# Optimization experiments

Measured on AMD Instinct MI355X. Metric: run time of the kernel, lower is better.

## Reference

```python
import jax, jax.numpy as jnp
import numpy as np

H = 32       # num query heads
KVH = 8      # num kv heads
HD = 64      # head_dim
ROPE_BASE = 10000.0


def _rope_cos_sin(seq_len, dtype):
    # inv_freq over half the head dim, emb = cat(freqs, freqs)
    inv_freq = 1.0 / (ROPE_BASE ** (jnp.arange(0, HD, 2, dtype=jnp.float32) / HD))
    t = jnp.arange(seq_len, dtype=jnp.float32)
    freqs = t[:, None] * inv_freq[None, :]          # (S, HD/2)
    emb = jnp.concatenate([freqs, freqs], axis=-1)  # (S, HD)
    return jnp.cos(emb).astype(dtype), jnp.sin(emb).astype(dtype)


def _rotate(x):
    x1, x2 = x[..., : HD // 2], x[..., HD // 2 :]
    return jnp.concatenate([-x2, x1], axis=-1)


def setup_inputs() -> dict:
    key = jax.random.key(0)
    ks = jax.random.split(key, 9)
    B, T, D = 2, 2048, 2048
    kv_dim = KVH * HD
    s = 0.02
    return {
        "x": jax.random.normal(ks[0], (B, T, D), jnp.float32),
        "Wq": jax.random.normal(ks[1], (D, D), jnp.float32) * s,
        "bq": jax.random.normal(ks[2], (D,), jnp.float32) * s,
        "Wk": jax.random.normal(ks[3], (kv_dim, D), jnp.float32) * s,
        "bk": jax.random.normal(ks[4], (kv_dim,), jnp.float32) * s,
        "Wv": jax.random.normal(ks[5], (kv_dim, D), jnp.float32) * s,
        "bv": jax.random.normal(ks[6], (kv_dim,), jnp.float32) * s,
        "Wo": jax.random.normal(ks[7], (D, D), jnp.float32) * s,
        "bo": jax.random.normal(ks[8], (D,), jnp.float32) * s,
    }


def reference(x, Wq, bq, Wk, bk, Wv, bv, Wo, bo):
    B, T, D = x.shape
    S = T  # self-attention, no KV cache (offset = 0)

    # QKV projections
    q = (x @ Wq.T + bq).reshape(B, T, H, HD)
    k = (x @ Wk.T + bk).reshape(B, S, KVH, HD)
    v = (x @ Wv.T + bv).reshape(B, S, KVH, HD)

    # RoPE (rotary dim == head_dim, offset 0)
    cos, sin = _rope_cos_sin(S, q.dtype)
    cos = cos[None, :, None, :]  # (1, S, 1, HD)
    sin = sin[None, :, None, :]
    q = q * cos + _rotate(q) * sin
    k = k * cos + _rotate(k) * sin

    # GQA: repeat kv heads (repeat_interleave along head dim)
    r = H // KVH
    k = jnp.repeat(k, r, axis=2)  # (B, S, H, HD)
    v = jnp.repeat(v, r, axis=2)

    # causal scaled dot-product attention
    scale = 1.0 / np.sqrt(HD)
    scores = jnp.einsum("bthd,bshd->bhts", q, k) * scale  # (B, H, T, S)
    causal = jnp.tril(jnp.ones((T, S), dtype=bool))
    scores = jnp.where(causal[None, None], scores, jnp.finfo(scores.dtype).min)
    probs = jax.nn.softmax(scores.astype(jnp.float32), axis=-1).astype(q.dtype)
    attn = jnp.einsum("bhts,bshd->bthd", probs, v)  # (B, T, H, HD)

    out = attn.reshape(B, T, H * HD) @ Wo.T + bo
    return out
```

## Files before the change

### kernel.cpp

```cpp
#include <hip/hip_runtime.h>
#include <hip/hip_bf16.h>
#include <cstdint>

#define B_ 2
#define T_ 2048
#define D_ 2048
#define H_ 32
#define KVH_ 8
#define HD_ 64
#define NQKV_ 3072
#define M_ 4096

typedef __attribute__((ext_vector_type(8))) __bf16 bf16x8;
typedef __attribute__((ext_vector_type(4))) float f32x4;
typedef __attribute__((ext_vector_type(4))) uint32_t u32x4;

__device__ __forceinline__ uint16_t f2bf(float f) {
  uint32_t u = __builtin_bit_cast(uint32_t, f);
  return (uint16_t)((u + 0x7FFFu + ((u >> 16) & 1u)) >> 16);
}

__device__ __forceinline__ uint32_t cvt_pk(float lo, float hi) {
  uint32_t r;
  asm("v_cvt_pk_bf16_f32 %0, %1, %2" : "=v"(r) : "v"(lo), "v"(hi));
  return r;
}

__device__ __forceinline__ void gload_lds16(const void* g, void* l) {
  __builtin_amdgcn_global_load_lds(
      (const __attribute__((address_space(1))) void*)(uintptr_t)g,
      (__attribute__((address_space(3))) void*)(uintptr_t)l, 16, 0, 0);
}

__global__ void cvt_bf16_k(const float* __restrict__ in, uint16_t* __restrict__ out, int n) {
  int i = (blockIdx.x * 256 + threadIdx.x) * 8;
  if (i >= n) return;
  float4 a = *reinterpret_cast<const float4*>(in + i);
  float4 b = *reinterpret_cast<const float4*>(in + i + 4);
  uint4 v;
  v.x = (uint32_t)f2bf(a.x) | ((uint32_t)f2bf(a.y) << 16);
  v.y = (uint32_t)f2bf(a.z) | ((uint32_t)f2bf(a.w) << 16);
  v.z = (uint32_t)f2bf(b.x) | ((uint32_t)f2bf(b.y) << 16);
  v.w = (uint32_t)f2bf(b.z) | ((uint32_t)f2bf(b.w) << 16);
  *reinterpret_cast<uint4*>(out + i) = v;
}

__global__ void concat_bias_k(const float* __restrict__ bq, const float* __restrict__ bk,
                              const float* __restrict__ bv, float* __restrict__ out) {
  int i = blockIdx.x * 256 + threadIdx.x;
  if (i >= NQKV_) return;
  out[i] = (i < D_) ? bq[i] : (i < D_ + 512) ? bk[i - D_] : bv[i - D_ - 512];
}

__global__ void rope_tab_k(float* __restrict__ cosT, float* __restrict__ sinT) {
  int i = blockIdx.x * 256 + threadIdx.x;
  int d = i & 31;
  int t = i >> 5;
  float inv = expf(-(float)d * (1.0f / 32.0f) * logf(10000.0f));
  float f = (float)t * inv;
  cosT[i] = cosf(f);
  sinT[i] = sinf(f);
}

#define BM 128
#define BN 128
#define BK 64
__global__ __launch_bounds__(256, 2)
void gemm_bf16(const uint16_t* __restrict__ A, const uint16_t* __restrict__ Bw,
               const float* __restrict__ bias, float* __restrict__ C,
               int M, int N, int K) {
  __shared__ __align__(16) uint16_t As[BM * BK];
  __shared__ __align__(16) uint16_t Bs[BN * BK];
  const int tid = threadIdx.x;
  const int lane = tid & 63;
  const int w = tid >> 6;
  const int wm = w >> 1, wn = w & 1;
  const int l16 = lane & 15, lq = lane >> 4;

  int lin = blockIdx.y * gridDim.x + blockIdx.x;
  int qn = (gridDim.x * gridDim.y) >> 3;
  int swz = (lin & 7) * qn + (lin >> 3);
  const int m0 = (swz / gridDim.x) * BM, n0 = (swz % gridDim.x) * BN;

  f32x4 acc[4][4] = {};

  for (int k0 = 0; k0 < K; k0 += BK) {
#pragma unroll
    for (int r = 0; r < 4; ++r) {
      int idx = r * 256 + tid;
      int row = idx >> 3;
      int c8 = (idx & 7) ^ (row & 7);
      gload_lds16(A + (size_t)(m0 + row) * K + k0 + c8 * 8, &As[idx * 8]);
    }
#pragma unroll
    for (int r = 0; r < 4; ++r) {
      int idx = r * 256 + tid;
      int row = idx >> 3;
      int c8 = (idx & 7) ^ (row & 7);
      gload_lds16(Bw + (size_t)(n0 + row) * K + k0 + c8 * 8, &Bs[idx * 8]);
    }
    __syncthreads();
#pragma unroll
    for (int ks = 0; ks < 2; ++ks) {
      bf16x8 av[4], bv[4];
      int k8 = ks * 4 + lq;
#pragma unroll
      for (int mi = 0; mi < 4; ++mi) {
        int row = wm * 64 + mi * 16 + l16;
        av[mi] = *reinterpret_cast<const bf16x8*>(&As[row * BK + ((k8 ^ (row & 7)) * 8)]);
      }
#pragma unroll
      for (int ni = 0; ni < 4; ++ni) {
        int row = wn * 64 + ni * 16 + l16;
        bv[ni] = *reinterpret_cast<const bf16x8*>(&Bs[row * BK + ((k8 ^ (row & 7)) * 8)]);
      }
#pragma unroll
      for (int mi = 0; mi < 4; ++mi)
#pragma unroll
        for (int ni = 0; ni < 4; ++ni)
          acc[mi][ni] = __builtin_amdgcn_mfma_f32_16x16x32_bf16(av[mi], bv[ni], acc[mi][ni], 0, 0, 0);
    }
    __syncthreads();
  }

#pragma unroll
  for (int mi = 0; mi < 4; ++mi) {
    int r0 = m0 + wm * 64 + mi * 16 + lq * 4;
#pragma unroll
    for (int ni = 0; ni < 4; ++ni) {
      int c = n0 + wn * 64 + ni * 16 + l16;
      float bb = bias[c];
#pragma unroll
      for (int rr = 0; rr < 4; ++rr)
        C[(size_t)(r0 + rr) * N + c] = acc[mi][ni][rr] + bb;
    }
  }
}

__global__ void rope_qk_k(const float* __restrict__ QKV, const float* __restrict__ cosT,
                          const float* __restrict__ sinT, uint16_t* __restrict__ qb,
                          uint16_t* __restrict__ kb) {
  int tid = blockIdx.x * 256 + threadIdx.x;
  int d = tid & 31;
  int t = (tid >> 5) & (T_ - 1);
  int rest = tid >> 16;
  int hh = rest % 40;
  int b = rest / 40;
  const float PREQ = 0.125f * 1.44269504f;
  float c = cosT[t * 32 + d];
  float s = sinT[t * 32 + d];
  size_t rowoff = (size_t)(b * T_ + t) * NQKV_;
  const int lq = d >> 3, e = d & 7;
  const int l16 = t & 15;
  const int lofs = (lq * 16 + l16) * 8 + e;
  if (hh < H_) {
    const float* q = QKV + rowoff + hh * 64;
    float x1 = q[d], x2 = q[d + 32];
    int tile = t >> 5, mf = (t >> 4) & 1;
    size_t base = ((size_t)(b * H_ + hh) * 64 + tile) * 2048;
    qb[base + (0 * 2 + mf) * 512 + lofs] = f2bf((x1 * c - x2 * s) * PREQ);
    qb[base + (1 * 2 + mf) * 512 + lofs] = f2bf((x2 * c + x1 * s) * PREQ);
  } else {
    int kh = hh - H_;
    const float* kp = QKV + rowoff + D_ + kh * 64;
    float x1 = kp[d], x2 = kp[d + 32];
    int it = t >> 6, nf = (t >> 4) & 3;
    size_t base = (size_t)(b * KVH_ + kh) * (T_ * HD_) + (size_t)it * 4096;
    kb[base + (0 * 8 + nf) * 512 + lofs] = f2bf(x1 * c - x2 * s);
    kb[base + (4 + nf) * 512 + lofs] = f2bf(x2 * c + x1 * s);
  }
}

__global__ void cvt_v_k(const float* __restrict__ QKV, uint16_t* __restrict__ vt) {
  int tid = blockIdx.x * 256 + threadIdx.x;
  int t8 = tid & 255;
  int rest = tid >> 8;
  int b = rest >> 9;
  int col = 2560 + (rest & 511);
  int d = rest & 63;
  int kvh = (rest >> 6) & 7;
  uint16_t tmp[8];
#pragma unroll
  for (int i = 0; i < 8; ++i)
    tmp[i] = f2bf(QKV[(size_t)(b * T_ + t8 * 8 + i) * NQKV_ + col]);
  uint4 v;
  v.x = (uint32_t)tmp[0] | ((uint32_t)tmp[1] << 16);
  v.y = (uint32_t)tmp[2] | ((uint32_t)tmp[3] << 16);
  v.z = (uint32_t)tmp[4] | ((uint32_t)tmp[5] << 16);
  v.w = (uint32_t)tmp[6] | ((uint32_t)tmp[7] << 16);
  int it = t8 >> 3, k2 = (t8 >> 2) & 1, lq = t8 & 3;
  int dn = d >> 4, l16 = d & 15;
  size_t base = (size_t)(b * KVH_ + kvh) * (T_ * HD_);
  *reinterpret_cast<uint4*>(vt + base + ((size_t)(it * 2 + k2) * 4 + dn) * 512 +
                            (lq * 16 + l16) * 8) = v;
}

__global__ __launch_bounds__(256, 2)
void flash_attn_k(const uint16_t* __restrict__ qb, const uint16_t* __restrict__ kb,
                  const uint16_t* __restrict__ vt, uint16_t* __restrict__ ob) {
  __shared__ __align__(16) uint16_t P_lds[4][32 * 72];
  const int lane = threadIdx.x & 63;
  const int w = threadIdx.x >> 6;
  const int l16 = lane & 15, lq = lane >> 4;
  const int bh = (blockIdx.x & 15) * 4 + w;
  const int rank = blockIdx.x >> 4;
  const int pair = rank & 31;
  const int tile = (rank & 32) ? (63 - pair) : pair;
  const int b = bh >> 5, h = bh & 31;
  const int kvh = h >> 2;
  uint16_t* P = P_lds[w];

  const uint16_t* Qp = qb + ((size_t)(b * H_ + h) * 64 + tile) * 2048;
  const uint16_t* Kp = kb + (size_t)(b * KVH_ + kvh) * (T_ * HD_);
  const uint16_t* Vp = vt + (size_t)(b * KVH_ + kvh) * (T_ * HD_);
  const int lofs = lane * 8;

  const int q0 = tile * 32;
  u32x4 ones_u = {0x3F803F80u, 0x3F803F80u, 0x3F803F80u, 0x3F803F80u};
  bf16x8 ones = __builtin_bit_cast(bf16x8, ones_u);

  bf16x8 aq[2][2];
#pragma unroll
  for (int mf = 0; mf < 2; ++mf)
#pragma unroll
    for (int ks = 0; ks < 2; ++ks)
      aq[mf][ks] = *reinterpret_cast<const bf16x8*>(Qp + (ks * 2 + mf) * 512 + lofs);

  f32x4 acc[2][4] = {};
  f32x4 acc_l[2] = {};

  const int nt = (tile >> 1) + 1;

  bf16x8 kA[2][4], kB[2][4];
#pragma unroll
  for (int ks = 0; ks < 2; ++ks)
#pragma unroll
    for (int nf = 0; nf < 4; ++nf)
      kA[ks][nf] = *reinterpret_cast<const bf16x8*>(Kp + (ks * 4 + nf) * 512 + lofs);

#define FLASH_STEP(KCUR, KNXT, IT)                                                     \
  do {                                                                                 \
    const int kv0 = (IT) * 64;                                                         \
    f32x4 sacc[4][2] = {};                                                             \
    _Pragma("unroll")                                                                  \
    for (int ks = 0; ks < 2; ++ks)                                                     \
      _Pragma("unroll")                                                                \
      for (int nf = 0; nf < 4; ++nf)                                                   \
        _Pragma("unroll")                                                              \
        for (int mf = 0; mf < 2; ++mf)                                                 \
          sacc[nf][mf] = __builtin_amdgcn_mfma_f32_16x16x32_bf16(                      \
              KCUR[ks][nf], aq[mf][ks], sacc[nf][mf], 0, 0, 0);                        \
    const int itn = ((IT) + 1 < nt) ? (IT) + 1 : (IT);                                 \
    _Pragma("unroll")                                                                  \
    for (int ks = 0; ks < 2; ++ks)                                                     \
      _Pragma("unroll")                                                                \
      for (int nf = 0; nf < 4; ++nf)                                                   \
        KNXT[ks][nf] = *reinterpret_cast<const bf16x8*>(                               \
            Kp + ((size_t)(itn * 2 + ks) * 4 + nf) * 512 + lofs);                      \
    bf16x8 vv[2][4];                                                                   \
    _Pragma("unroll")                                                                  \
    for (int k2 = 0; k2 < 2; ++k2)                                                     \
      _Pragma("unroll")                                                                \
      for (int dn = 0; dn < 4; ++dn)                                                   \
        vv[k2][dn] = *reinterpret_cast<const bf16x8*>(                                 \
            Vp + ((size_t)((IT) * 2 + k2) * 4 + dn) * 512 + lofs);                     \
    if ((IT) == nt - 1) {                                                              \
      _Pragma("unroll")                                                                \
      for (int mf = 0; mf < 2; ++mf) {                                                 \
        int qg = q0 + mf * 16 + l16;                                                   \
        _Pragma("unroll")                                                              \
        for (int nf = 0; nf < 4; ++nf)                                                 \
          _Pragma("unroll")                                                            \
          for (int r = 0; r < 4; ++r)                                                  \
            if (kv0 + nf * 16 + lq * 4 + r > qg) sacc[nf][mf][r] = -1e30f;             \
      }                                                                                \
    }                                                                                  \
    _Pragma("unroll")                                                                  \
    for (int mf = 0; mf < 2; ++mf) {                                                   \
      uint16_t* rowp = P + (mf * 16 + l16) * 72;                                       \
      _Pragma("unroll")                                                                \
      for (int nf = 0; nf < 4; ++nf) {                                                 \
        float p0 = __builtin_amdgcn_exp2f(sacc[nf][mf][0]);                            \
        float p1 = __builtin_amdgcn_exp2f(sacc[nf][mf][1]);                            \
        float p2 = __builtin_amdgcn_exp2f(sacc[nf][mf][2]);                            \
        float p3 = __builtin_amdgcn_exp2f(sacc[nf][mf][3]);                            \
        uint2 pk;                                                                      \
        pk.x = cvt_pk(p0, p1);                                                         \
        pk.y = cvt_pk(p2, p3);                                                         \
        *reinterpret_cast<uint2*>(rowp + nf * 16 + lq * 4) = pk;                       \
      }                                                                                \
    }                                                                                  \
    bf16x8 pa[2][2];                                                                   \
    _Pragma("unroll")                                                                  \
    for (int mf = 0; mf < 2; ++mf)                                                     \
      _Pragma("unroll")                                                                \
      for (int k2 = 0; k2 < 2; ++k2)                                                   \
        pa[mf][k2] = *reinterpret_cast<const bf16x8*>(                                 \
            P + (mf * 16 + l16) * 72 + k2 * 32 + lq * 8);                              \
    _Pragma("unroll")                                                                  \
    for (int k2 = 0; k2 < 2; ++k2)                                                     \
      _Pragma("unroll")                                                                \
      for (int mf = 0; mf < 2; ++mf) {                                                 \
        acc_l[mf] = __builtin_amdgcn_mfma_f32_16x16x32_bf16(ones, pa[mf][k2],          \
                                                            acc_l[mf], 0, 0, 0);      \
        _Pragma("unroll")                                                              \
        for (int dn = 0; dn < 4; ++dn)                                                 \
          acc[mf][dn] = __builtin_amdgcn_mfma_f32_16x16x32_bf16(                       \
              vv[k2][dn], pa[mf][k2], acc[mf][dn], 0, 0, 0);                           \
      }                                                                                \
  } while (0)

  {
    int it = 0;
    for (;;) {
      FLASH_STEP(kA, kB, it);
      ++it;
      if (it == nt) break;
      FLASH_STEP(kB, kA, it);
      ++it;
      if (it == nt) break;
    }
  }
#undef FLASH_STEP

#pragma unroll
  for (int mf = 0; mf < 2; ++mf) {
    float inv = 1.0f / acc_l[mf][0];
    uint16_t* rowp = P + (mf * 16 + l16) * 72;
#pragma unroll
    for (int dn = 0; dn < 4; ++dn) {
      uint2 pk;
      pk.x = cvt_pk(acc[mf][dn][0] * inv, acc[mf][dn][1] * inv);
      pk.y = cvt_pk(acc[mf][dn][2] * inv, acc[mf][dn][3] * inv);
      *reinterpret_cast<uint2*>(rowp + dn * 16 + lq * 4) = pk;
    }
  }
  {
    int orow = lane >> 1, ohalf = (lane & 1) * 32;
    uint16_t* op = ob + (size_t)(b * T_ + q0 + orow) * D_ + h * HD_ + ohalf;
    const uint16_t* lp = P + orow * 72 + ohalf;
#pragma unroll
    for (int j = 0; j < 4; ++j)
      *reinterpret_cast<uint4*>(op + j * 8) = *reinterpret_cast<const uint4*>(lp + j * 8);
  }
}

extern "C" void kernel_launch(void* const* d_in, const int* in_sizes, int n_in,
                              void* d_out, int out_size, void* d_ws, size_t ws_size,
                              hipStream_t stream) {
  const float* x  = (const float*)d_in[0];
  const float* Wq = (const float*)d_in[1];
  const float* bq = (const float*)d_in[2];
  const float* Wk = (const float*)d_in[3];
  const float* bk = (const float*)d_in[4];
  const float* Wv = (const float*)d_in[5];
  const float* bv = (const float*)d_in[6];
  const float* Wo = (const float*)d_in[7];
  const float* bo = (const float*)d_in[8];
  float* out = (float*)d_out;

  char* ws = (char*)d_ws;
  size_t off = 0;
  auto alloc = [&](size_t bytes) {
    void* p = ws + off;
    off += (bytes + 255) & ~(size_t)255;
    return p;
  };
  uint16_t* xb    = (uint16_t*)alloc((size_t)M_ * D_ * 2);
  uint16_t* wqkv  = (uint16_t*)alloc((size_t)NQKV_ * D_ * 2);
  uint16_t* wo_b  = (uint16_t*)alloc((size_t)D_ * D_ * 2);
  float*    bqkv  = (float*)alloc(NQKV_ * 4);
  float*    cosT  = (float*)alloc(T_ * 32 * 4);
  float*    sinT  = (float*)alloc(T_ * 32 * 4);
  uint16_t* q_bf  = (uint16_t*)alloc((size_t)B_ * H_ * T_ * HD_ * 2);
  uint16_t* k_bf  = (uint16_t*)alloc((size_t)B_ * KVH_ * T_ * HD_ * 2);
  uint16_t* vt_bf = (uint16_t*)alloc((size_t)B_ * KVH_ * T_ * HD_ * 2);
  float*    qkvf  = (float*)alloc((size_t)M_ * NQKV_ * 4);
  uint16_t* attn_bf = (uint16_t*)qkvf;

  cvt_bf16_k<<<4096, 256, 0, stream>>>(x, xb, M_ * D_);
  cvt_bf16_k<<<2048, 256, 0, stream>>>(Wq, wqkv, D_ * D_);
  cvt_bf16_k<<<512, 256, 0, stream>>>(Wk, wqkv + (size_t)D_ * D_, 512 * D_);
  cvt_bf16_k<<<512, 256, 0, stream>>>(Wv, wqkv + (size_t)2560 * D_, 512 * D_);
  cvt_bf16_k<<<2048, 256, 0, stream>>>(Wo, wo_b, D_ * D_);
  concat_bias_k<<<12, 256, 0, stream>>>(bq, bk, bv, bqkv);
  rope_tab_k<<<256, 256, 0, stream>>>(cosT, sinT);

  gemm_bf16<<<dim3(NQKV_ / BN, M_ / BM), 256, 0, stream>>>(xb, wqkv, bqkv, qkvf, M_, NQKV_, D_);

  rope_qk_k<<<(B_ * 40 * T_ * 32) / 256, 256, 0, stream>>>(qkvf, cosT, sinT, q_bf, k_bf);
  cvt_v_k<<<(B_ * KVH_ * HD_ * (T_ / 8)) / 256, 256, 0, stream>>>(qkvf, vt_bf);

  flash_attn_k<<<1024, 256, 0, stream>>>(q_bf, k_bf, vt_bf, attn_bf);

  gemm_bf16<<<dim3(D_ / BN, M_ / BM), 256, 0, stream>>>(attn_bf, wo_b, bo, out, M_, D_, D_);
}
```

Before: 206.4 us.

## Replace GEMM with 256x256 double-buffered LDS kernel using 8 waves

Both projection GEMMs now use a new kernel with 256x256 output tiles, 512 threads and a double-buffered LDS stage. The next K-tile is prefetched while the current one is consumed, with interleaved barriers and raised wave priority around the MFMA bursts. The goal is to hide global-load latency and increase operand reuse per LDS byte. The trade-off is 128 KB of LDS per block and far fewer blocks: 192 and 128, against 256 CUs. That may leave CUs idle, especially for the output projection.

```diff
diff --git a/kernel.cpp b/kernel.cpp
--- a/kernel.cpp
+++ b/kernel.cpp
@@ -62,70 +62,101 @@
   sinT[i] = sinf(f);
 }
 
-#define BM 128
-#define BN 128
-#define BK 64
-__global__ __launch_bounds__(256, 2)
-void gemm_bf16(const uint16_t* __restrict__ A, const uint16_t* __restrict__ Bw,
-               const float* __restrict__ bias, float* __restrict__ C,
-               int M, int N, int K) {
-  __shared__ __align__(16) uint16_t As[BM * BK];
-  __shared__ __align__(16) uint16_t Bs[BN * BK];
+#define GBM 256
+#define GBN 256
+#define GBK 64
+__global__ __launch_bounds__(512, 2)
+void gemm256(const uint16_t* __restrict__ A, const uint16_t* __restrict__ Bw,
+             const float* __restrict__ bias, float* __restrict__ C,
+             int M, int N, int K) {
+  __shared__ __align__(16) uint16_t lds[2][2][GBM * GBK];
   const int tid = threadIdx.x;
   const int lane = tid & 63;
   const int w = tid >> 6;
-  const int wm = w >> 1, wn = w & 1;
+  const int wm = w >> 2, wn = w & 3;
   const int l16 = lane & 15, lq = lane >> 4;
 
   int lin = blockIdx.y * gridDim.x + blockIdx.x;
   int qn = (gridDim.x * gridDim.y) >> 3;
   int swz = (lin & 7) * qn + (lin >> 3);
-  const int m0 = (swz / gridDim.x) * BM, n0 = (swz % gridDim.x) * BN;
-
-  f32x4 acc[4][4] = {};
-
-  for (int k0 = 0; k0 < K; k0 += BK) {
-#pragma unroll
-    for (int r = 0; r < 4; ++r) {
-      int idx = r * 256 + tid;
-      int row = idx >> 3;
-      int c8 = (idx & 7) ^ (row & 7);
-      gload_lds16(A + (size_t)(m0 + row) * K + k0 + c8 * 8, &As[idx * 8]);
-    }
-#pragma unroll
-    for (int r = 0; r < 4; ++r) {
-      int idx = r * 256 + tid;
-      int row = idx >> 3;
-      int c8 = (idx & 7) ^ (row & 7);
-      gload_lds16(Bw + (size_t)(n0 + row) * K + k0 + c8 * 8, &Bs[idx * 8]);
-    }
-    __syncthreads();
-#pragma unroll
-    for (int ks = 0; ks < 2; ++ks) {
-      bf16x8 av[4], bv[4];
-      int k8 = ks * 4 + lq;
-#pragma unroll
-      for (int mi = 0; mi < 4; ++mi) {
-        int row = wm * 64 + mi * 16 + l16;
-        av[mi] = *reinterpret_cast<const bf16x8*>(&As[row * BK + ((k8 ^ (row & 7)) * 8)]);
+  const int m0 = (swz / gridDim.x) * GBM, n0 = (swz % gridDim.x) * GBN;
+
+  auto stage = [&](int dbuf, int kt) {
+    int k0 = kt * GBK;
+#pragma unroll
+    for (int j = 0; j < 4; ++j) {
+      int off = w * 4096 + j * 1024 + lane * 16;
+      int row = off >> 7;
+      int colb = (off & 127) ^ ((row & 7) << 4);
+      gload_lds16(A + (size_t)(m0 + row) * K + k0 + (colb >> 1),
+                  (char*)&lds[dbuf][0][0] + off);
+    }
+#pragma unroll
+    for (int j = 0; j < 4; ++j) {
+      int off = w * 4096 + j * 1024 + lane * 16;
+      int row = off >> 7;
+      int colb = (off & 127) ^ ((row & 7) << 4);
+      gload_lds16(Bw + (size_t)(n0 + row) * K + k0 + (colb >> 1),
+                  (char*)&lds[dbuf][1][0] + off);
+    }
+  };
+
+  f32x4 acc[8][4] = {};
+  const int NT = K / GBK;
+
+  stage(0, 0);
+  asm volatile("s_waitcnt vmcnt(0)" ::: "memory");
+  __builtin_amdgcn_s_barrier();
+
+  for (int t = 0; t < NT; ++t) {
+    const int cur = t & 1;
+    const char* Ab = (const char*)&lds[cur][0][0];
+    const char* Bb = (const char*)&lds[cur][1][0];
+
+    stage(cur ^ 1, (t + 1 < NT) ? t + 1 : 0);
+
+    bf16x8 bfr[4][2];
+#pragma unroll
+    for (int ni = 0; ni < 4; ++ni)
+#pragma unroll
+      for (int ks = 0; ks < 2; ++ks) {
+        int R = wn * 64 + ni * 16 + l16;
+        int colb = (ks * 64 + lq * 16) ^ ((R & 7) << 4);
+        bfr[ni][ks] = *reinterpret_cast<const bf16x8*>(Bb + R * 128 + colb);
       }
-#pragma unroll
-      for (int ni = 0; ni < 4; ++ni) {
-        int row = wn * 64 + ni * 16 + l16;
-        bv[ni] = *reinterpret_cast<const bf16x8*>(&Bs[row * BK + ((k8 ^ (row & 7)) * 8)]);
-      }
-#pragma unroll
-      for (int mi = 0; mi < 4; ++mi)
-#pragma unroll
-        for (int ni = 0; ni < 4; ++ni)
-          acc[mi][ni] = __builtin_amdgcn_mfma_f32_16x16x32_bf16(av[mi], bv[ni], acc[mi][ni], 0, 0, 0);
-    }
-    __syncthreads();
-  }
-
-#pragma unroll
-  for (int mi = 0; mi < 4; ++mi) {
-    int r0 = m0 + wm * 64 + mi * 16 + lq * 4;
+
+#pragma unroll
+    for (int q = 0; q < 4; ++q) {
+      bf16x8 afr[2][2];
+#pragma unroll
+      for (int mi2 = 0; mi2 < 2; ++mi2)
+#pragma unroll
+        for (int ks = 0; ks < 2; ++ks) {
+          int R = wm * 128 + (q * 2 + mi2) * 16 + l16;
+          int colb = (ks * 64 + lq * 16) ^ ((R & 7) << 4);
+          afr[mi2][ks] = *reinterpret_cast<const bf16x8*>(Ab + R * 128 + colb);
+        }
+      if (q == 3) asm volatile("s_waitcnt vmcnt(0)" ::: "memory");
+      __builtin_amdgcn_s_barrier();
+      asm volatile("s_waitcnt lgkmcnt(0)" ::: "memory");
+      __builtin_amdgcn_sched_barrier(0);
+      __builtin_amdgcn_s_setprio(1);
+#pragma unroll
+      for (int ks = 0; ks < 2; ++ks)
+#pragma unroll
+        for (int mi2 = 0; mi2 < 2; ++mi2)
+#pragma unroll
+          for (int ni = 0; ni < 4; ++ni)
+            acc[q * 2 + mi2][ni] = __builtin_amdgcn_mfma_f32_16x16x32_bf16(
+                afr[mi2][ks], bfr[ni][ks], acc[q * 2 + mi2][ni], 0, 0, 0);
+      __builtin_amdgcn_s_setprio(0);
+      __builtin_amdgcn_s_barrier();
+    }
+  }
+
+#pragma unroll
+  for (int mi = 0; mi < 8; ++mi) {
+    int r0 = m0 + wm * 128 + mi * 16 + lq * 4;
 #pragma unroll
     for (int ni = 0; ni < 4; ++ni) {
       int c = n0 + wn * 64 + ni * 16 + l16;
@@ -386,12 +417,12 @@
   concat_bias_k<<<12, 256, 0, stream>>>(bq, bk, bv, bqkv);
   rope_tab_k<<<256, 256, 0, stream>>>(cosT, sinT);
 
-  gemm_bf16<<<dim3(NQKV_ / BN, M_ / BM), 256, 0, stream>>>(xb, wqkv, bqkv, qkvf, M_, NQKV_, D_);
+  gemm256<<<dim3(NQKV_ / GBN, M_ / GBM), 512, 0, stream>>>(xb, wqkv, bqkv, qkvf, M_, NQKV_, D_);
 
   rope_qk_k<<<(B_ * 40 * T_ * 32) / 256, 256, 0, stream>>>(qkvf, cosT, sinT, q_bf, k_bf);
   cvt_v_k<<<(B_ * KVH_ * HD_ * (T_ / 8)) / 256, 256, 0, stream>>>(qkvf, vt_bf);
 
   flash_attn_k<<<1024, 256, 0, stream>>>(q_bf, k_bf, vt_bf, attn_bf);
 
-  gemm_bf16<<<dim3(D_ / BN, M_ / BM), 256, 0, stream>>>(attn_bf, wo_b, bo, out, M_, D_, D_);
-}
+  gemm256<<<dim3(D_ / GBN, M_ / GBM), 512, 0, stream>>>(attn_bf, wo_b, bo, out, M_, D_, D_);
+}
```

After: 232.3 us (median of 4 runs). 1.13x slower.
